# Kernel tuning notes

Measured on AMD Instinct MI355X. Metric: run time of the kernel, lower is better.

## Reference

```python
import jax, jax.numpy as jnp
import numpy as np

N = 100000      # nodes
F_IN = 256      # num_node_features
E = 1600000     # edges (before self-loops)
DIMS = [F_IN, 128, 100, 32, 2]  # GCNConv layer widths


def _glorot(key, fan_in, fan_out):
    s = jnp.sqrt(6.0 / (fan_in + fan_out))
    return jax.random.uniform(key, (fan_in, fan_out), jnp.float32, -s, s)


def setup_inputs() -> dict:
    key = jax.random.key(0)
    ks = jax.random.split(key, 10)
    x = jax.random.normal(ks[0], (N, F_IN), jnp.float32)
    edge_index = jax.random.randint(ks[1], (2, E), 0, N, jnp.int32)
    inp = {"x": x, "edge_index": edge_index}
    for i in range(4):
        inp[f"W{i+1}"] = _glorot(ks[2 + 2 * i], DIMS[i], DIMS[i + 1])
        inp[f"b{i+1}"] = jnp.zeros((DIMS[i + 1],), jnp.float32)
    return inp


def reference(x, edge_index, W1, b1, W2, b2, W3, b3, W4, b4):
    n = x.shape[0]
    loops = jnp.arange(n, dtype=edge_index.dtype)
    src = jnp.concatenate([edge_index[0], loops])  # [E+N]
    dst = jnp.concatenate([edge_index[1], loops])
    # symmetric normalization: deg^-1/2[src] * deg^-1/2[dst] (self-loops included)
    deg = jax.ops.segment_sum(jnp.ones_like(src, x.dtype), dst, num_segments=n)
    dis = jax.lax.rsqrt(jnp.maximum(deg, 1.0))
    norm = (dis[src] * dis[dst])[:, None]  # [E+N, 1]

    def conv(h, W, b):
        h = h @ W                                      # [N, out]
        msg = h[src] * norm                            # gather + scale [E+N, out]
        return jax.ops.segment_sum(msg, dst, num_segments=n) + b

    h = jax.nn.leaky_relu(conv(x, W1, b1), negative_slope=0.1)
    h = jax.nn.leaky_relu(conv(h, W2, b2), negative_slope=0.1)
    h = jax.nn.leaky_relu(conv(h, W3, b3), negative_slope=0.1)
    h = conv(h, W4, b4)
    return jax.nn.softmax(h, axis=-1)
```

## Files before the change

kernel.cpp:

```cpp
#include <hip/hip_runtime.h>
#include <math.h>


typedef unsigned short ushort_t;
typedef unsigned int   uint_t;
typedef short  bf16x8 __attribute__((ext_vector_type(8)));
typedef float  f32x4  __attribute__((ext_vector_type(4)));

#define BKT_SHIFT 8
#define BKT_CAP   5120
#define BIN_CHUNK 4096

__device__ __forceinline__ ushort_t f2bf(float f) {
    union { float f; uint_t u; } v; v.f = f;
    uint_t u = v.u;
    u += 0x7fffu + ((u >> 16) & 1u);
    return (ushort_t)(u >> 16);
}
__device__ __forceinline__ float bflo(uint_t u) {
    union { uint_t q; float f; } v; v.q = u << 16; return v.f;
}
__device__ __forceinline__ float bfhi(uint_t u) {
    union { uint_t q; float f; } v; v.q = u & 0xffff0000u; return v.f;
}


__global__ __launch_bounds__(256) void bin_kernel(const int* __restrict__ srcArr,
                                                  const int* __restrict__ dstArr,
                                                  int* __restrict__ bkt_cursor,
                                                  uint2* __restrict__ staging,
                                                  int E, int nb) {
    __shared__ int hist[512];
    __shared__ int base[512];
    for (int b = threadIdx.x; b < 512; b += 256) hist[b] = 0;
    __syncthreads();
    const int e0 = blockIdx.x * BIN_CHUNK;
    #pragma unroll 4
    for (int k = 0; k < BIN_CHUNK / 256; ++k) {
        int e = e0 + k * 256 + threadIdx.x;
        if (e < E) atomicAdd(&hist[dstArr[e] >> BKT_SHIFT], 1);
    }
    __syncthreads();
    for (int b = threadIdx.x; b < nb; b += 256) {
        int h = hist[b];
        base[b] = h ? atomicAdd(&bkt_cursor[b], h) : 0;
    }
    __syncthreads();
    for (int b = threadIdx.x; b < 512; b += 256) hist[b] = 0;
    __syncthreads();
    #pragma unroll 4
    for (int k = 0; k < BIN_CHUNK / 256; ++k) {
        int e = e0 + k * 256 + threadIdx.x;
        if (e < E) {
            int s = srcArr[e], d = dstArr[e];
            int b = d >> BKT_SHIFT;
            int p = atomicAdd(&hist[b], 1);
            int idx = base[b] + p;
            if (idx < BKT_CAP)
                staging[(size_t)b * BKT_CAP + idx] = make_uint2((uint_t)s, (uint_t)d);
        }
    }
}

__global__ __launch_bounds__(256) void deg_from_staging_kernel(const uint2* __restrict__ staging,
                                                               const int* __restrict__ bkt_cursor,
                                                               int* __restrict__ degi, int n) {
    __shared__ int cur[256];
    const int b  = blockIdx.x;
    const int lo = b << BKT_SHIFT;
    const int nl = min(256, n - lo);
    cur[threadIdx.x] = 0;
    __syncthreads();
    int cnt = min(bkt_cursor[b], BKT_CAP);
    for (int e = threadIdx.x; e < cnt; e += 256) {
        uint2 p = staging[(size_t)b * BKT_CAP + e];
        atomicAdd(&cur[(int)p.y - lo], 1);
    }
    __syncthreads();
    if ((int)threadIdx.x < nl) degi[lo + threadIdx.x] = cur[threadIdx.x];
}

__global__ void dis_kernel(const int* __restrict__ degi, float* __restrict__ dis, int n) {
    int i = blockIdx.x * blockDim.x + threadIdx.x;
    if (i < n) dis[i] = rsqrtf((float)(degi[i] + 1));
}

__global__ void scan_block_kernel(const int* __restrict__ degi, int* __restrict__ row_excl,
                                  int* __restrict__ bsums, int n) {
    __shared__ int buf[1024];
    int i = blockIdx.x * 1024 + threadIdx.x;
    int v = (i < n) ? degi[i] : 0;
    buf[threadIdx.x] = v;
    __syncthreads();
    for (int off = 1; off < 1024; off <<= 1) {
        int t = (threadIdx.x >= (unsigned)off) ? buf[threadIdx.x - off] : 0;
        __syncthreads();
        buf[threadIdx.x] += t;
        __syncthreads();
    }
    if (i < n) row_excl[i] = buf[threadIdx.x] - v;
    if (threadIdx.x == 1023) bsums[blockIdx.x] = buf[1023];
}

__global__ void scan_sums_kernel(int* __restrict__ bsums, int nb) {
    __shared__ int buf[128];
    int v = ((int)threadIdx.x < nb) ? bsums[threadIdx.x] : 0;
    buf[threadIdx.x] = v;
    __syncthreads();
    for (int off = 1; off < 128; off <<= 1) {
        int t = (threadIdx.x >= (unsigned)off) ? buf[threadIdx.x - off] : 0;
        __syncthreads();
        buf[threadIdx.x] += t;
        __syncthreads();
    }
    if ((int)threadIdx.x < nb) bsums[threadIdx.x] = buf[threadIdx.x] - v;
    if (threadIdx.x == 0) bsums[nb] = buf[127];
}

__global__ void scan_add_kernel(int* __restrict__ row_start, const int* __restrict__ bsums,
                                int n, int nb) {
    int i = blockIdx.x * blockDim.x + threadIdx.x;
    if (i < n) row_start[i] += bsums[i >> 10];
    else if (i == n) row_start[n] = bsums[nb];
}

__global__ __launch_bounds__(256) void csr_build_kernel(const uint2* __restrict__ staging,
                                                        const int* __restrict__ bkt_cursor,
                                                        const int* __restrict__ row_start,
                                                        int* __restrict__ csr_src, int n) {
    __shared__ int rs[257];
    __shared__ int cur[256];
    __shared__ int seg[BKT_CAP];
    const int b  = blockIdx.x;
    const int lo = b << BKT_SHIFT;
    const int nl = min(256, n - lo);
    if ((int)threadIdx.x <= nl) rs[threadIdx.x] = row_start[lo + threadIdx.x];
    cur[threadIdx.x] = 0;
    __syncthreads();
    const int sbase = rs[0];
    int cnt = min(bkt_cursor[b], BKT_CAP);
    for (int e = threadIdx.x; e < cnt; e += 256) {
        uint2 p = staging[(size_t)b * BKT_CAP + e];
        int ln = (int)p.y - lo;
        int q  = atomicAdd(&cur[ln], 1);
        seg[(rs[ln] - sbase) + q] = (int)p.x;
    }
    __syncthreads();
    for (int i = threadIdx.x; i < cnt; i += 256) csr_src[sbase + i] = seg[i];
}


__global__ void wt_kernel(const float* __restrict__ W, ushort_t* __restrict__ Wt,
                          int K, int N, int KP, int NP) {
    int idx = blockIdx.x * blockDim.x + threadIdx.x;
    if (idx >= KP * NP) return;
    int n = idx / KP, k = idx % KP;
    float v = (k < K && n < N) ? W[(size_t)k * N + n] : 0.f;
    Wt[(size_t)n * KP + k] = f2bf(v);
}

template <bool A_FP32>
__global__ __launch_bounds__(256) void mfma_gemm(const void* __restrict__ Av,
                                                 const ushort_t* __restrict__ Bt,
                                                 ushort_t* __restrict__ C,
                                                 int M, int K, int lda, int ldb,
                                                 int ldc, int nstore) {
    __shared__ __attribute__((aligned(16))) ushort_t As[128][72];
    __shared__ __attribute__((aligned(16))) ushort_t Bs[64][72];

    const int t    = threadIdx.x;
    const int lane = t & 63;
    const int w    = t >> 6;
    const int wm   = w >> 1, wn = w & 1;
    const int m0   = blockIdx.x * 128;
    const int n0   = blockIdx.y * 64;

    f32x4 acc[4][2];
    #pragma unroll
    for (int mi = 0; mi < 4; ++mi)
        #pragma unroll
        for (int ni = 0; ni < 2; ++ni) acc[mi][ni] = (f32x4){0.f, 0.f, 0.f, 0.f};

    const int srow = t >> 3;
    const int scol = (t & 7) * 8;

    for (int k0 = 0; k0 < K; k0 += 64) {
        #pragma unroll
        for (int it = 0; it < 4; ++it) {
            int r = srow + it * 32;
            int gm = m0 + r;
            bf16x8 v = {0, 0, 0, 0, 0, 0, 0, 0};
            if (gm < M) {
                if (A_FP32) {
                    const float* A = (const float*)Av;
                    const float4 f0 = *(const float4*)(A + (size_t)gm * lda + k0 + scol);
                    const float4 f1 = *(const float4*)(A + (size_t)gm * lda + k0 + scol + 4);
                    ushort_t o[8] = { f2bf(f0.x), f2bf(f0.y), f2bf(f0.z), f2bf(f0.w),
                                      f2bf(f1.x), f2bf(f1.y), f2bf(f1.z), f2bf(f1.w) };
                    v = *(const bf16x8*)o;
                } else {
                    const ushort_t* A = (const ushort_t*)Av;
                    v = *(const bf16x8*)(A + (size_t)gm * lda + k0 + scol);
                }
            }
            *(bf16x8*)&As[r][scol] = v;
        }
        #pragma unroll
        for (int it = 0; it < 2; ++it) {
            int r = srow + it * 32;
            bf16x8 v = *(const bf16x8*)(Bt + (size_t)(n0 + r) * ldb + k0 + scol);
            *(bf16x8*)&Bs[r][scol] = v;
        }
        __syncthreads();
        #pragma unroll
        for (int kk = 0; kk < 2; ++kk) {
            bf16x8 af[4], bfr[2];
            const int kc = kk * 32 + (lane >> 4) * 8;
            #pragma unroll
            for (int mi = 0; mi < 4; ++mi)
                af[mi] = *(const bf16x8*)&As[wm * 64 + mi * 16 + (lane & 15)][kc];
            #pragma unroll
            for (int ni = 0; ni < 2; ++ni)
                bfr[ni] = *(const bf16x8*)&Bs[wn * 32 + ni * 16 + (lane & 15)][kc];
            #pragma unroll
            for (int mi = 0; mi < 4; ++mi)
                #pragma unroll
                for (int ni = 0; ni < 2; ++ni)
                    acc[mi][ni] = __builtin_amdgcn_mfma_f32_16x16x32_bf16(
                        af[mi], bfr[ni], acc[mi][ni], 0, 0, 0);
        }
        __syncthreads();
    }

    #pragma unroll
    for (int mi = 0; mi < 4; ++mi)
        #pragma unroll
        for (int ni = 0; ni < 2; ++ni)
            #pragma unroll
            for (int r = 0; r < 4; ++r) {
                int gm = m0 + wm * 64 + mi * 16 + (lane >> 4) * 4 + r;
                int gn = n0 + wn * 32 + ni * 16 + (lane & 15);
                if (gm < M && gn < nstore)
                    C[(size_t)gm * ldc + gn] = f2bf(acc[mi][ni][r]);
            }
}

template <int F>
__global__ void aggregate128_kernel(const ushort_t* __restrict__ h, const int* __restrict__ row_start,
                                    const int* __restrict__ csr_src,
                                    const float* __restrict__ dis, const float* __restrict__ bias,
                                    ushort_t* __restrict__ out, int n) {
    int wid  = threadIdx.x >> 6;
    int lane = threadIdx.x & 63;
    int node = blockIdx.x * (blockDim.x >> 6) + wid;
    if (node >= n) return;
    const int f0 = 2 * lane, f1 = f0 + 1;
    float dn = dis[node];
    uint_t v = *(const uint_t*)(h + (size_t)node * 128 + f0);
    float acc0 = bflo(v) * dn;
    float acc1 = bfhi(v) * dn;
    int i = row_start[node], end = row_start[node + 1];
    for (; i + 4 <= end; i += 4) {
        int s0 = csr_src[i], s1 = csr_src[i + 1], s2 = csr_src[i + 2], s3 = csr_src[i + 3];
        float m0 = dis[s0], m1 = dis[s1], m2 = dis[s2], m3 = dis[s3];
        uint_t u0 = *(const uint_t*)(h + (size_t)s0 * 128 + f0);
        uint_t u1 = *(const uint_t*)(h + (size_t)s1 * 128 + f0);
        uint_t u2 = *(const uint_t*)(h + (size_t)s2 * 128 + f0);
        uint_t u3 = *(const uint_t*)(h + (size_t)s3 * 128 + f0);
        acc0 += bflo(u0) * m0; acc1 += bfhi(u0) * m0;
        acc0 += bflo(u1) * m1; acc1 += bfhi(u1) * m1;
        acc0 += bflo(u2) * m2; acc1 += bfhi(u2) * m2;
        acc0 += bflo(u3) * m3; acc1 += bfhi(u3) * m3;
    }
    for (; i < end; ++i) {
        int s = csr_src[i];
        float nrm = dis[s];
        uint_t u = *(const uint_t*)(h + (size_t)s * 128 + f0);
        acc0 += bflo(u) * nrm; acc1 += bfhi(u) * nrm;
    }
    acc0 = acc0 * dn + ((f0 < F) ? bias[f0] : 0.f);
    acc1 = acc1 * dn + ((f1 < F) ? bias[f1] : 0.f);
    acc0 = (acc0 > 0.f) ? acc0 : 0.1f * acc0;
    acc1 = (acc1 > 0.f) ? acc1 : 0.1f * acc1;
    if (f0 >= F) acc0 = 0.f;
    if (f1 >= F) acc1 = 0.f;
    uint_t o = (uint_t)f2bf(acc0) | ((uint_t)f2bf(acc1) << 16);
    *(uint_t*)(out + (size_t)node * 128 + f0) = o;
}

__global__ void aggregate32_kernel(const ushort_t* __restrict__ h, const int* __restrict__ row_start,
                                   const int* __restrict__ csr_src,
                                   const float* __restrict__ dis, const float* __restrict__ bias,
                                   ushort_t* __restrict__ out, int n) {
    int lane16 = threadIdx.x & 15;
    int node = blockIdx.x * (blockDim.x >> 4) + (threadIdx.x >> 4);
    if (node >= n) return;
    const int f0 = 2 * lane16;
    float dn = dis[node];
    uint_t v = *(const uint_t*)(h + (size_t)node * 32 + f0);
    float acc0 = bflo(v) * dn;
    float acc1 = bfhi(v) * dn;
    int i = row_start[node], end = row_start[node + 1];
    for (; i + 4 <= end; i += 4) {
        int s0 = csr_src[i], s1 = csr_src[i + 1], s2 = csr_src[i + 2], s3 = csr_src[i + 3];
        float m0 = dis[s0], m1 = dis[s1], m2 = dis[s2], m3 = dis[s3];
        uint_t u0 = *(const uint_t*)(h + (size_t)s0 * 32 + f0);
        uint_t u1 = *(const uint_t*)(h + (size_t)s1 * 32 + f0);
        uint_t u2 = *(const uint_t*)(h + (size_t)s2 * 32 + f0);
        uint_t u3 = *(const uint_t*)(h + (size_t)s3 * 32 + f0);
        acc0 += bflo(u0) * m0; acc1 += bfhi(u0) * m0;
        acc0 += bflo(u1) * m1; acc1 += bfhi(u1) * m1;
        acc0 += bflo(u2) * m2; acc1 += bfhi(u2) * m2;
        acc0 += bflo(u3) * m3; acc1 += bfhi(u3) * m3;
    }
    for (; i < end; ++i) {
        int s = csr_src[i];
        float nrm = dis[s];
        uint_t u = *(const uint_t*)(h + (size_t)s * 32 + f0);
        acc0 += bflo(u) * nrm; acc1 += bfhi(u) * nrm;
    }
    acc0 = acc0 * dn + bias[f0];
    acc1 = acc1 * dn + bias[f0 + 1];
    acc0 = (acc0 > 0.f) ? acc0 : 0.1f * acc0;
    acc1 = (acc1 > 0.f) ? acc1 : 0.1f * acc1;
    uint_t o = (uint_t)f2bf(acc0) | ((uint_t)f2bf(acc1) << 16);
    *(uint_t*)(out + (size_t)node * 32 + f0) = o;
}

__global__ void gemm32x2_kernel(const ushort_t* __restrict__ H, const float* __restrict__ W4,
                                float* __restrict__ C, int n) {
    int node = blockIdx.x * blockDim.x + threadIdx.x;
    if (node >= n) return;
    const uint_t* row = (const uint_t*)(H + (size_t)node * 32);
    float a0 = 0.f, a1 = 0.f;
    #pragma unroll
    for (int k2 = 0; k2 < 16; ++k2) {
        uint_t u = row[k2];
        float x0 = bflo(u), x1 = bfhi(u);
        int k = 2 * k2;
        a0 += x0 * W4[k * 2]     + x1 * W4[(k + 1) * 2];
        a1 += x0 * W4[k * 2 + 1] + x1 * W4[(k + 1) * 2 + 1];
    }
    C[2 * (size_t)node] = a0;
    C[2 * (size_t)node + 1] = a1;
}

__global__ void aggregate2_softmax_kernel(const float* __restrict__ h, const int* __restrict__ row_start,
                                          const int* __restrict__ csr_src,
                                          const float* __restrict__ dis, const float* __restrict__ bias,
                                          float* __restrict__ out, int n) {
    int node = blockIdx.x * blockDim.x + threadIdx.x;
    if (node >= n) return;
    float dn = dis[node];
    float a0 = h[2 * (size_t)node]     * dn;
    float a1 = h[2 * (size_t)node + 1] * dn;
    int beg = row_start[node], end = row_start[node + 1];
    for (int i = beg; i < end; ++i) {
        int s = csr_src[i];
        float nrm = dis[s];
        a0 += h[2 * (size_t)s]     * nrm;
        a1 += h[2 * (size_t)s + 1] * nrm;
    }
    a0 = a0 * dn + bias[0];
    a1 = a1 * dn + bias[1];
    float m  = fmaxf(a0, a1);
    float e0 = expf(a0 - m), e1 = expf(a1 - m);
    float inv = 1.f / (e0 + e1);
    out[2 * (size_t)node]     = e0 * inv;
    out[2 * (size_t)node + 1] = e1 * inv;
}


extern "C" void kernel_launch(void* const* d_in, const int* in_sizes, int n_in,
                              void* d_out, int out_size, void* d_ws, size_t ws_size,
                              hipStream_t stream) {
    const float* x  = (const float*)d_in[0];
    const int*   ei = (const int*)d_in[1];
    const float* W1 = (const float*)d_in[2];
    const float* b1 = (const float*)d_in[3];
    const float* W2 = (const float*)d_in[4];
    const float* b2 = (const float*)d_in[5];
    const float* W3 = (const float*)d_in[6];
    const float* b3 = (const float*)d_in[7];
    const float* W4 = (const float*)d_in[8];
    const float* b4 = (const float*)d_in[9];

    const int N = in_sizes[0] / 256;
    const int E = in_sizes[1] / 2;
    const int* srcA = ei;
    const int* dstA = ei + E;
    const int nbkt = (N + 255) >> BKT_SHIFT;

    char* ws = (char*)d_ws;
    size_t off = 0;
    auto alloc = [&](size_t bytes) {
        void* p = ws + off;
        off = (off + bytes + 255) & ~(size_t)255;
        return p;
    };
    int*      degi       = (int*)alloc((size_t)N * 4);
    float*    dis        = (float*)alloc((size_t)N * 4);
    int*      row_start  = (int*)alloc((size_t)(N + 1) * 4);
    int*      bsums      = (int*)alloc(512 * 4);
    int*      bkt_cursor = (int*)alloc((size_t)nbkt * 4);
    int*      csr_src    = (int*)alloc((size_t)E * 4);
    uint2*    staging    = (uint2*)alloc((size_t)nbkt * BKT_CAP * 8);
    ushort_t* bufA       = (ushort_t*)alloc((size_t)N * 128 * 2);
    ushort_t* bufB       = (ushort_t*)alloc((size_t)N * 128 * 2);
    float*    C4         = (float*)alloc((size_t)N * 2 * 4);
    ushort_t* Wt1        = (ushort_t*)alloc((size_t)128 * 256 * 2);
    ushort_t* Wt2        = (ushort_t*)alloc((size_t)128 * 128 * 2);
    ushort_t* Wt3        = (ushort_t*)alloc((size_t)64 * 128 * 2);
    (void)ws_size;

    hipMemsetAsync(bkt_cursor, 0, (size_t)nbkt * 4, stream);

    bin_kernel<<<(E + BIN_CHUNK - 1) / BIN_CHUNK, 256, 0, stream>>>(
        srcA, dstA, bkt_cursor, staging, E, nbkt);
    deg_from_staging_kernel<<<nbkt, 256, 0, stream>>>(staging, bkt_cursor, degi, N);
    dis_kernel<<<(N + 255) / 256, 256, 0, stream>>>(degi, dis, N);
    const int nb = (N + 1023) >> 10;
    scan_block_kernel<<<nb, 1024, 0, stream>>>(degi, row_start, bsums, N);
    scan_sums_kernel<<<1, 128, 0, stream>>>(bsums, nb);
    scan_add_kernel<<<(N + 256) / 256, 256, 0, stream>>>(row_start, bsums, N, nb);
    csr_build_kernel<<<nbkt, 256, 0, stream>>>(staging, bkt_cursor, row_start, csr_src, N);

    wt_kernel<<<(256 * 128 + 255) / 256, 256, 0, stream>>>(W1, Wt1, 256, 128, 256, 128);
    wt_kernel<<<(128 * 128 + 255) / 256, 256, 0, stream>>>(W2, Wt2, 128, 100, 128, 128);
    wt_kernel<<<(128 * 64 + 255) / 256, 256, 0, stream>>>(W3, Wt3, 100, 32, 128, 64);

    const int gx = (N + 127) / 128;
    const int aggBlocks128 = (N + 3) / 4;
    const int aggBlocks32  = (N + 15) / 16;

    mfma_gemm<true><<<dim3(gx, 2), 256, 0, stream>>>(x, Wt1, bufA, N, 256, 256, 256, 128, 128);
    aggregate128_kernel<128><<<aggBlocks128, 256, 0, stream>>>(
        bufA, row_start, csr_src, dis, b1, bufB, N);
    mfma_gemm<false><<<dim3(gx, 2), 256, 0, stream>>>(bufB, Wt2, bufA, N, 128, 128, 128, 128, 128);
    aggregate128_kernel<100><<<aggBlocks128, 256, 0, stream>>>(
        bufA, row_start, csr_src, dis, b2, bufB, N);
    mfma_gemm<false><<<dim3(gx, 1), 256, 0, stream>>>(bufB, Wt3, bufA, N, 128, 128, 128, 32, 32);
    aggregate32_kernel<<<aggBlocks32, 256, 0, stream>>>(
        bufA, row_start, csr_src, dis, b3, bufB, N);
    gemm32x2_kernel<<<(N + 255) / 256, 256, 0, stream>>>(bufB, W4, C4, N);
    aggregate2_softmax_kernel<<<(N + 255) / 256, 256, 0, stream>>>(
        C4, row_start, csr_src, dis, b4, (float*)d_out, N);
}
```

Measured before the change: 335.0 us.

## Prescale GEMM outputs by source norm and split aggregate edges across half-waves

The source-side degree normalization is folded into the GEMM epilogues, so the aggregation kernels no longer gather dis[src] per edge and only scale by dis[node] at the end. The 128-wide aggregation now has each half-wave process alternate edges with 4-feature vector loads, then combines the halves with a shuffle. dis computation is fused into the degree kernel, and the three weight-transpose launches are merged into one. This removes a random per-edge gather and some launches, at the cost of a bf16 rounding of the prescaled features and half the wave idle in the epilogue.

```diff
diff --git a/kernel.cpp b/kernel.cpp
--- a/kernel.cpp
+++ b/kernel.cpp
@@ -64,7 +64,8 @@
 
 __global__ __launch_bounds__(256) void deg_from_staging_kernel(const uint2* __restrict__ staging,
                                                                const int* __restrict__ bkt_cursor,
-                                                               int* __restrict__ degi, int n) {
+                                                               int* __restrict__ degi,
+                                                               float* __restrict__ dis, int n) {
     __shared__ int cur[256];
     const int b  = blockIdx.x;
     const int lo = b << BKT_SHIFT;
@@ -77,12 +78,11 @@
         atomicAdd(&cur[(int)p.y - lo], 1);
     }
     __syncthreads();
-    if ((int)threadIdx.x < nl) degi[lo + threadIdx.x] = cur[threadIdx.x];
-}
-
-__global__ void dis_kernel(const int* __restrict__ degi, float* __restrict__ dis, int n) {
-    int i = blockIdx.x * blockDim.x + threadIdx.x;
-    if (i < n) dis[i] = rsqrtf((float)(degi[i] + 1));
+    if ((int)threadIdx.x < nl) {
+        int d = cur[threadIdx.x];
+        degi[lo + threadIdx.x] = d;
+        dis[lo + threadIdx.x] = rsqrtf((float)(d + 1));
+    }
 }
 
 __global__ void scan_block_kernel(const int* __restrict__ degi, int* __restrict__ row_excl,
@@ -149,20 +149,32 @@
     for (int i = threadIdx.x; i < cnt; i += 256) csr_src[sbase + i] = seg[i];
 }
 
-
-__global__ void wt_kernel(const float* __restrict__ W, ushort_t* __restrict__ Wt,
-                          int K, int N, int KP, int NP) {
+__global__ void wt_all_kernel(const float* __restrict__ W1, const float* __restrict__ W2,
+                              const float* __restrict__ W3,
+                              ushort_t* __restrict__ Wt1, ushort_t* __restrict__ Wt2,
+                              ushort_t* __restrict__ Wt3) {
     int idx = blockIdx.x * blockDim.x + threadIdx.x;
-    if (idx >= KP * NP) return;
-    int n = idx / KP, k = idx % KP;
-    float v = (k < K && n < N) ? W[(size_t)k * N + n] : 0.f;
-    Wt[(size_t)n * KP + k] = f2bf(v);
+    if (idx < 32768) {
+        int nn = idx >> 8, k = idx & 255;
+        Wt1[idx] = f2bf(W1[(size_t)k * 128 + nn]);
+    } else if (idx < 49152) {
+        int j = idx - 32768;
+        int nn = j >> 7, k = j & 127;
+        float v = (nn < 100) ? W2[(size_t)k * 100 + nn] : 0.f;
+        Wt2[j] = f2bf(v);
+    } else if (idx < 57344) {
+        int j = idx - 49152;
+        int nn = j >> 7, k = j & 127;
+        float v = (k < 100 && nn < 32) ? W3[(size_t)k * 32 + nn] : 0.f;
+        Wt3[j] = f2bf(v);
+    }
 }
 
 template <bool A_FP32>
 __global__ __launch_bounds__(256) void mfma_gemm(const void* __restrict__ Av,
                                                  const ushort_t* __restrict__ Bt,
                                                  ushort_t* __restrict__ C,
+                                                 const float* __restrict__ dis,
                                                  int M, int K, int lda, int ldb,
                                                  int ldc, int nstore) {
     __shared__ __attribute__((aligned(16))) ushort_t As[128][72];
@@ -235,14 +247,17 @@
     #pragma unroll
     for (int mi = 0; mi < 4; ++mi)
         #pragma unroll
-        for (int ni = 0; ni < 2; ++ni)
+        for (int r = 0; r < 4; ++r) {
+            int gm = m0 + wm * 64 + mi * 16 + (lane >> 4) * 4 + r;
+            if (gm >= M) continue;
+            float d = dis[gm];
             #pragma unroll
-            for (int r = 0; r < 4; ++r) {
-                int gm = m0 + wm * 64 + mi * 16 + (lane >> 4) * 4 + r;
+            for (int ni = 0; ni < 2; ++ni) {
                 int gn = n0 + wn * 32 + ni * 16 + (lane & 15);
-                if (gm < M && gn < nstore)
-                    C[(size_t)gm * ldc + gn] = f2bf(acc[mi][ni][r]);
+                if (gn < nstore)
+                    C[(size_t)gm * ldc + gn] = f2bf(acc[mi][ni][r] * d);
             }
+        }
 }
 
 template <int F>
@@ -254,38 +269,57 @@
     int lane = threadIdx.x & 63;
     int node = blockIdx.x * (blockDim.x >> 6) + wid;
     if (node >= n) return;
-    const int f0 = 2 * lane, f1 = f0 + 1;
-    float dn = dis[node];
-    uint_t v = *(const uint_t*)(h + (size_t)node * 128 + f0);
-    float acc0 = bflo(v) * dn;
-    float acc1 = bfhi(v) * dn;
+    const int half = lane >> 5;
+    const int fb   = (lane & 31) * 4;
+    float a0 = 0.f, a1 = 0.f, a2 = 0.f, a3 = 0.f;
     int i = row_start[node], end = row_start[node + 1];
-    for (; i + 4 <= end; i += 4) {
-        int s0 = csr_src[i], s1 = csr_src[i + 1], s2 = csr_src[i + 2], s3 = csr_src[i + 3];
-        float m0 = dis[s0], m1 = dis[s1], m2 = dis[s2], m3 = dis[s3];
-        uint_t u0 = *(const uint_t*)(h + (size_t)s0 * 128 + f0);
-        uint_t u1 = *(const uint_t*)(h + (size_t)s1 * 128 + f0);
-        uint_t u2 = *(const uint_t*)(h + (size_t)s2 * 128 + f0);
-        uint_t u3 = *(const uint_t*)(h + (size_t)s3 * 128 + f0);
-        acc0 += bflo(u0) * m0; acc1 += bfhi(u0) * m0;
-        acc0 += bflo(u1) * m1; acc1 += bfhi(u1) * m1;
-        acc0 += bflo(u2) * m2; acc1 += bfhi(u2) * m2;
-        acc0 += bflo(u3) * m3; acc1 += bfhi(u3) * m3;
-    }
-    for (; i < end; ++i) {
-        int s = csr_src[i];
-        float nrm = dis[s];
-        uint_t u = *(const uint_t*)(h + (size_t)s * 128 + f0);
-        acc0 += bflo(u) * nrm; acc1 += bfhi(u) * nrm;
-    }
-    acc0 = acc0 * dn + ((f0 < F) ? bias[f0] : 0.f);
-    acc1 = acc1 * dn + ((f1 < F) ? bias[f1] : 0.f);
-    acc0 = (acc0 > 0.f) ? acc0 : 0.1f * acc0;
-    acc1 = (acc1 > 0.f) ? acc1 : 0.1f * acc1;
-    if (f0 >= F) acc0 = 0.f;
-    if (f1 >= F) acc1 = 0.f;
-    uint_t o = (uint_t)f2bf(acc0) | ((uint_t)f2bf(acc1) << 16);
-    *(uint_t*)(out + (size_t)node * 128 + f0) = o;
+    const int cnt = end - i;
+    for (; i + 8 <= end; i += 8) {
+        int s0 = csr_src[i     + half];
+        int s1 = csr_src[i + 2 + half];
+        int s2 = csr_src[i + 4 + half];
+        int s3 = csr_src[i + 6 + half];
+        uint2 u0 = *(const uint2*)(h + (size_t)s0 * 128 + fb);
+        uint2 u1 = *(const uint2*)(h + (size_t)s1 * 128 + fb);
+        uint2 u2 = *(const uint2*)(h + (size_t)s2 * 128 + fb);
+        uint2 u3 = *(const uint2*)(h + (size_t)s3 * 128 + fb);
+        a0 += bflo(u0.x); a1 += bfhi(u0.x); a2 += bflo(u0.y); a3 += bfhi(u0.y);
+        a0 += bflo(u1.x); a1 += bfhi(u1.x); a2 += bflo(u1.y); a3 += bfhi(u1.y);
+        a0 += bflo(u2.x); a1 += bfhi(u2.x); a2 += bflo(u2.y); a3 += bfhi(u2.y);
+        a0 += bflo(u3.x); a1 += bfhi(u3.x); a2 += bflo(u3.y); a3 += bfhi(u3.y);
+    }
+    for (; i + 2 <= end; i += 2) {
+        int s = csr_src[i + half];
+        uint2 u = *(const uint2*)(h + (size_t)s * 128 + fb);
+        a0 += bflo(u.x); a1 += bfhi(u.x); a2 += bflo(u.y); a3 += bfhi(u.y);
+    }
+    if ((cnt & 1) && half == 0) {
+        int s = csr_src[end - 1];
+        uint2 u = *(const uint2*)(h + (size_t)s * 128 + fb);
+        a0 += bflo(u.x); a1 += bfhi(u.x); a2 += bflo(u.y); a3 += bfhi(u.y);
+    }
+    a0 += __shfl_xor(a0, 32);
+    a1 += __shfl_xor(a1, 32);
+    a2 += __shfl_xor(a2, 32);
+    a3 += __shfl_xor(a3, 32);
+    if (half == 0) {
+        uint2 u = *(const uint2*)(h + (size_t)node * 128 + fb);
+        a0 += bflo(u.x); a1 += bfhi(u.x); a2 += bflo(u.y); a3 += bfhi(u.y);
+        float dn = dis[node];
+        float b0 = 0.f, b1 = 0.f, b2 = 0.f, b3 = 0.f;
+        if (fb < F) { float4 bv = *(const float4*)(bias + fb); b0 = bv.x; b1 = bv.y; b2 = bv.z; b3 = bv.w; }
+        a0 = a0 * dn + b0;  a1 = a1 * dn + b1;
+        a2 = a2 * dn + b2;  a3 = a3 * dn + b3;
+        a0 = (a0 > 0.f) ? a0 : 0.1f * a0;
+        a1 = (a1 > 0.f) ? a1 : 0.1f * a1;
+        a2 = (a2 > 0.f) ? a2 : 0.1f * a2;
+        a3 = (a3 > 0.f) ? a3 : 0.1f * a3;
+        if (fb >= F) { a0 = 0.f; a1 = 0.f; a2 = 0.f; a3 = 0.f; }
+        uint2 o;
+        o.x = (uint_t)f2bf(a0) | ((uint_t)f2bf(a1) << 16);
+        o.y = (uint_t)f2bf(a2) | ((uint_t)f2bf(a3) << 16);
+        *(uint2*)(out + (size_t)node * 128 + fb) = o;
+    }
 }
 
 __global__ void aggregate32_kernel(const ushort_t* __restrict__ h, const int* __restrict__ row_start,
@@ -296,29 +330,25 @@
     int node = blockIdx.x * (blockDim.x >> 4) + (threadIdx.x >> 4);
     if (node >= n) return;
     const int f0 = 2 * lane16;
-    float dn = dis[node];
     uint_t v = *(const uint_t*)(h + (size_t)node * 32 + f0);
-    float acc0 = bflo(v) * dn;
-    float acc1 = bfhi(v) * dn;
+    float acc0 = bflo(v);
+    float acc1 = bfhi(v);
     int i = row_start[node], end = row_start[node + 1];
     for (; i + 4 <= end; i += 4) {
         int s0 = csr_src[i], s1 = csr_src[i + 1], s2 = csr_src[i + 2], s3 = csr_src[i + 3];
-        float m0 = dis[s0], m1 = dis[s1], m2 = dis[s2], m3 = dis[s3];
         uint_t u0 = *(const uint_t*)(h + (size_t)s0 * 32 + f0);
         uint_t u1 = *(const uint_t*)(h + (size_t)s1 * 32 + f0);
         uint_t u2 = *(const uint_t*)(h + (size_t)s2 * 32 + f0);
         uint_t u3 = *(const uint_t*)(h + (size_t)s3 * 32 + f0);
-        acc0 += bflo(u0) * m0; acc1 += bfhi(u0) * m0;
-        acc0 += bflo(u1) * m1; acc1 += bfhi(u1) * m1;
-        acc0 += bflo(u2) * m2; acc1 += bfhi(u2) * m2;
-        acc0 += bflo(u3) * m3; acc1 += bfhi(u3) * m3;
+        acc0 += bflo(u0) + bflo(u1) + bflo(u2) + bflo(u3);
+        acc1 += bfhi(u0) + bfhi(u1) + bfhi(u2) + bfhi(u3);
     }
     for (; i < end; ++i) {
         int s = csr_src[i];
-        float nrm = dis[s];
         uint_t u = *(const uint_t*)(h + (size_t)s * 32 + f0);
-        acc0 += bflo(u) * nrm; acc1 += bfhi(u) * nrm;
-    }
+        acc0 += bflo(u); acc1 += bfhi(u);
+    }
+    float dn = dis[node];
     acc0 = acc0 * dn + bias[f0];
     acc1 = acc1 * dn + bias[f0 + 1];
     acc0 = (acc0 > 0.f) ? acc0 : 0.1f * acc0;
@@ -328,7 +358,7 @@
 }
 
 __global__ void gemm32x2_kernel(const ushort_t* __restrict__ H, const float* __restrict__ W4,
-                                float* __restrict__ C, int n) {
+                                const float* __restrict__ dis, float* __restrict__ C, int n) {
     int node = blockIdx.x * blockDim.x + threadIdx.x;
     if (node >= n) return;
     const uint_t* row = (const uint_t*)(H + (size_t)node * 32);
@@ -341,8 +371,9 @@
         a0 += x0 * W4[k * 2]     + x1 * W4[(k + 1) * 2];
         a1 += x0 * W4[k * 2 + 1] + x1 * W4[(k + 1) * 2 + 1];
     }
-    C[2 * (size_t)node] = a0;
-    C[2 * (size_t)node + 1] = a1;
+    float d = dis[node];
+    C[2 * (size_t)node]     = a0 * d;
+    C[2 * (size_t)node + 1] = a1 * d;
 }
 
 __global__ void aggregate2_softmax_kernel(const float* __restrict__ h, const int* __restrict__ row_start,
@@ -351,16 +382,15 @@
                                           float* __restrict__ out, int n) {
     int node = blockIdx.x * blockDim.x + threadIdx.x;
     if (node >= n) return;
-    float dn = dis[node];
-    float a0 = h[2 * (size_t)node]     * dn;
-    float a1 = h[2 * (size_t)node + 1] * dn;
+    float a0 = h[2 * (size_t)node];
+    float a1 = h[2 * (size_t)node + 1];
     int beg = row_start[node], end = row_start[node + 1];
     for (int i = beg; i < end; ++i) {
         int s = csr_src[i];
-        float nrm = dis[s];
-        a0 += h[2 * (size_t)s]     * nrm;
-        a1 += h[2 * (size_t)s + 1] * nrm;
-    }
+        a0 += h[2 * (size_t)s];
+        a1 += h[2 * (size_t)s + 1];
+    }
+    float dn = dis[node];
     a0 = a0 * dn + bias[0];
     a1 = a1 * dn + bias[1];
     float m  = fmaxf(a0, a1);
@@ -417,32 +447,29 @@
 
     bin_kernel<<<(E + BIN_CHUNK - 1) / BIN_CHUNK, 256, 0, stream>>>(
         srcA, dstA, bkt_cursor, staging, E, nbkt);
-    deg_from_staging_kernel<<<nbkt, 256, 0, stream>>>(staging, bkt_cursor, degi, N);
-    dis_kernel<<<(N + 255) / 256, 256, 0, stream>>>(degi, dis, N);
+    deg_from_staging_kernel<<<nbkt, 256, 0, stream>>>(staging, bkt_cursor, degi, dis, N);
     const int nb = (N + 1023) >> 10;
     scan_block_kernel<<<nb, 1024, 0, stream>>>(degi, row_start, bsums, N);
     scan_sums_kernel<<<1, 128, 0, stream>>>(bsums, nb);
     scan_add_kernel<<<(N + 256) / 256, 256, 0, stream>>>(row_start, bsums, N, nb);
     csr_build_kernel<<<nbkt, 256, 0, stream>>>(staging, bkt_cursor, row_start, csr_src, N);
 
-    wt_kernel<<<(256 * 128 + 255) / 256, 256, 0, stream>>>(W1, Wt1, 256, 128, 256, 128);
-    wt_kernel<<<(128 * 128 + 255) / 256, 256, 0, stream>>>(W2, Wt2, 128, 100, 128, 128);
-    wt_kernel<<<(128 * 64 + 255) / 256, 256, 0, stream>>>(W3, Wt3, 100, 32, 128, 64);
+    wt_all_kernel<<<(57344 + 255) / 256, 256, 0, stream>>>(W1, W2, W3, Wt1, Wt2, Wt3);
 
     const int gx = (N + 127) / 128;
     const int aggBlocks128 = (N + 3) / 4;
     const int aggBlocks32  = (N + 15) / 16;
 
-    mfma_gemm<true><<<dim3(gx, 2), 256, 0, stream>>>(x, Wt1, bufA, N, 256, 256, 256, 128, 128);
+    mfma_gemm<true><<<dim3(gx, 2), 256, 0, stream>>>(x, Wt1, bufA, dis, N, 256, 256, 256, 128, 128);
     aggregate128_kernel<128><<<aggBlocks128, 256, 0, stream>>>(
         bufA, row_start, csr_src, dis, b1, bufB, N);
-    mfma_gemm<false><<<dim3(gx, 2), 256, 0, stream>>>(bufB, Wt2, bufA, N, 128, 128, 128, 128, 128);
+    mfma_gemm<false><<<dim3(gx, 2), 256, 0, stream>>>(bufB, Wt2, bufA, dis, N, 128, 128, 128, 128, 128);
     aggregate128_kernel<100><<<aggBlocks128, 256, 0, stream>>>(
         bufA, row_start, csr_src, dis, b2, bufB, N);
-    mfma_gemm<false><<<dim3(gx, 1), 256, 0, stream>>>(bufB, Wt3, bufA, N, 128, 128, 128, 32, 32);
+    mfma_gemm<false><<<dim3(gx, 1), 256, 0, stream>>>(bufB, Wt3, bufA, dis, N, 128, 128, 128, 32, 32);
     aggregate32_kernel<<<aggBlocks32, 256, 0, stream>>>(
         bufA, row_start, csr_src, dis, b3, bufB, N);
-    gemm32x2_kernel<<<(N + 255) / 256, 256, 0, stream>>>(bufB, W4, C4, N);
+    gemm32x2_kernel<<<(N + 255) / 256, 256, 0, stream>>>(bufB, W4, dis, C4, N);
     aggregate2_softmax_kernel<<<(N + 255) / 256, 256, 0, stream>>>(
         C4, row_start, csr_src, dis, b4, (float*)d_out, N);
 }
```

Measured after the change: 321.5 us. 4.0% less time.
